# Kernel tuning notes

Measured on AMD Instinct MI355X. Metric: run time of the kernel, lower is better.

Reference implementation:

```python
import jax, jax.numpy as jnp
import numpy as np

D_IN = 256
DIMS = 256


def setup_inputs() -> dict:
    key = jax.random.key(0)
    k1, k2, k3, k4, k5 = jax.random.split(key, 5)
    B, Tq, Tk = 4, 512, 512
    query = jax.random.normal(k1, (B, Tq, D_IN), dtype=jnp.float32)
    value = jax.random.normal(k2, (B, Tk, D_IN), dtype=jnp.float32)
    # Dense(dims, use_bias=False) kernels (glorot-like scale) and AdditiveAttention scale vector
    Wq = jax.random.normal(k3, (D_IN, DIMS), dtype=jnp.float32) / np.sqrt(D_IN)
    Wv = jax.random.normal(k4, (D_IN, DIMS), dtype=jnp.float32) / np.sqrt(D_IN)
    scale = jax.random.normal(k5, (DIMS,), dtype=jnp.float32)
    return {"query": query, "value": value, "Wq": Wq, "Wv": Wv, "scale": scale}


def reference(query, value, Wq, Wv, scale):
    # q_proj: [B,Tq,d], k_proj: [B,Tk,d]; attention value = RAW value tensor (as in source)
    q = jnp.einsum("bqi,id->bqd", query, Wq)
    k = jnp.einsum("bki,id->bkd", value, Wv)
    # Additive (Bahdanau) scores: [B,Tq,Tk] via broadcast tanh then reduce with scale
    scores = jnp.einsum("bqkd,d->bqk", jnp.tanh(q[:, :, None, :] + k[:, None, :, :]), scale)
    attn = jax.nn.softmax(scores, axis=-1)  # masks are all-ones -> no-op
    out = jnp.einsum("bqk,bki->bqi", attn, value)
    return out, attn
```

## Files before the change

### kernel.cpp

```cpp
#include <hip/hip_runtime.h>

#define LOG2E 1.4426950408889634f
#define TWO_LOG2E 2.885390081777927f

__device__ __forceinline__ float fast_exp2(float x) { return __builtin_amdgcn_exp2f(x); }
__device__ __forceinline__ float fast_rcp(float x)  { return __builtin_amdgcn_rcpf(x); }

__device__ __forceinline__ void term2(float s0, float s1, float qx, float qy,
                                      float kx, float ky, float& acc) {
    const float A = fmaf(qx, kx, 1.f);
    const float B = fmaf(qy, ky, 1.f);
    acc = fmaf(fmaf(s1, A, s0 * B), fast_rcp(A * B), acc);
}

__global__ __launch_bounds__(256) void proj_kernel(
    const float* __restrict__ query, const float* __restrict__ value,
    const float* __restrict__ Wq, const float* __restrict__ Wv,
    float* __restrict__ eq, float* __restrict__ ek)
{
    __shared__ float in_lds[8 * 256];
    const int t = threadIdx.x;
    const int row0 = blockIdx.x * 8;
    const float* src; const float* W; float* dst;
    if (row0 < 2048) { src = query + (size_t)row0 * 256; W = Wq; dst = eq + (size_t)row0 * 256; }
    else { const int r = row0 - 2048; src = value + (size_t)r * 256; W = Wv; dst = ek + (size_t)r * 256; }

    const float4* s4 = (const float4*)src;
    float4* l4 = (float4*)in_lds;
    l4[t] = s4[t];
    l4[t + 256] = s4[t + 256];
    __syncthreads();

    float acc[8];
#pragma unroll
    for (int r = 0; r < 8; ++r) acc[r] = 0.f;

    for (int d = 0; d < 256; d += 4) {
        const float w0 = W[(d + 0) * 256 + t];
        const float w1 = W[(d + 1) * 256 + t];
        const float w2 = W[(d + 2) * 256 + t];
        const float w3 = W[(d + 3) * 256 + t];
#pragma unroll
        for (int r = 0; r < 8; ++r) {
            const float4 v = *(const float4*)&in_lds[r * 256 + d];
            acc[r] = fmaf(v.x, w0, acc[r]);
            acc[r] = fmaf(v.y, w1, acc[r]);
            acc[r] = fmaf(v.z, w2, acc[r]);
            acc[r] = fmaf(v.w, w3, acc[r]);
        }
    }
#pragma unroll
    for (int r = 0; r < 8; ++r) dst[r * 256 + t] = fast_exp2(acc[r] * TWO_LOG2E);
}

#define EK_ST 260
#define EQ_ST 260
#define SS_ST 520
#define PS_ST 520
__global__ __launch_bounds__(1024) void fused_kernel(
    const float* __restrict__ eq, const float* __restrict__ ek,
    const float* __restrict__ scale, const float* __restrict__ value,
    float* __restrict__ attn, float* __restrict__ out)
{
    __shared__ float ek_lds[64 * EK_ST];
    __shared__ float eq_lds[8 * EQ_ST];
    __shared__ float sc_lds[256];
    __shared__ float s_tile[8 * SS_ST];
    __shared__ float pslot[8 * PS_ST];
    __shared__ float inv_lds[8];

    const int t = threadIdx.x;
    const int w = t >> 6, lane = t & 63;
    const int oct = w >> 1, qh = w & 1;
    const int dd = lane >> 5, qp = (lane >> 4) & 1, kq = lane & 15;
    const int qt = blockIdx.x, b = blockIdx.y;
    const int q0 = qt * 8;

    const float4* ekb4 = (const float4*)(ek + (size_t)(b * 512) * 256);

    if (t < 512) {
        const int row = t >> 6, c = t & 63;
        const float4 v = ((const float4*)(eq + (size_t)(b * 512 + q0) * 256))[row * 64 + c];
        *(float4*)&eq_lds[row * EQ_ST + 4 * c] = v;
    } else if (t < 768) {
        sc_lds[t - 512] = -2.f * scale[t - 512];
    }
    {
#pragma unroll
        for (int l = 0; l < 4; ++l) {
            const int row = w + 16 * l;
            const int cc = (lane + (row >> 2)) & 63;
            *(float4*)&ek_lds[row * EK_ST + 4 * cc] = ekb4[(size_t)row * 64 + lane];
        }
    }
    __syncthreads();

    const int qr0 = 4 * qh + 2 * qp;
    const float* eqr0 = &eq_lds[(qr0 + 0) * EQ_ST];
    const float* eqr1 = &eq_lds[(qr0 + 1) * EQ_ST];

    for (int tt = 0; tt < 8; ++tt) {
        float a00 = 0.f, a01 = 0.f, a02 = 0.f, a03 = 0.f;
        float a10 = 0.f, a11 = 0.f, a12 = 0.f, a13 = 0.f;

#pragma unroll
        for (int it = 0; it < 4; ++it) {
            const int d = 32 * oct + 16 * dd + 4 * it;
            const float4 sv  = *(const float4*)&sc_lds[d];
            const float4 q0v = *(const float4*)&eqr0[d];
            const float4 q1v = *(const float4*)&eqr1[d];
            const int cc = 4 * (((d >> 2) + kq) & 63);
            const float4 k0 = *(const float4*)&ek_lds[(4 * kq + 0) * EK_ST + cc];
            const float4 k1 = *(const float4*)&ek_lds[(4 * kq + 1) * EK_ST + cc];
            const float4 k2 = *(const float4*)&ek_lds[(4 * kq + 2) * EK_ST + cc];
            const float4 k3 = *(const float4*)&ek_lds[(4 * kq + 3) * EK_ST + cc];

            term2(sv.x, sv.y, q0v.x, q0v.y, k0.x, k0.y, a00);
            term2(sv.x, sv.y, q0v.x, q0v.y, k1.x, k1.y, a01);
            term2(sv.x, sv.y, q0v.x, q0v.y, k2.x, k2.y, a02);
            term2(sv.x, sv.y, q0v.x, q0v.y, k3.x, k3.y, a03);
            term2(sv.x, sv.y, q1v.x, q1v.y, k0.x, k0.y, a10);
            term2(sv.x, sv.y, q1v.x, q1v.y, k1.x, k1.y, a11);
            term2(sv.x, sv.y, q1v.x, q1v.y, k2.x, k2.y, a12);
            term2(sv.x, sv.y, q1v.x, q1v.y, k3.x, k3.y, a13);

            term2(sv.z, sv.w, q0v.z, q0v.w, k0.z, k0.w, a00);
            term2(sv.z, sv.w, q0v.z, q0v.w, k1.z, k1.w, a01);
            term2(sv.z, sv.w, q0v.z, q0v.w, k2.z, k2.w, a02);
            term2(sv.z, sv.w, q0v.z, q0v.w, k3.z, k3.w, a03);
            term2(sv.z, sv.w, q1v.z, q1v.w, k0.z, k0.w, a10);
            term2(sv.z, sv.w, q1v.z, q1v.w, k1.z, k1.w, a11);
            term2(sv.z, sv.w, q1v.z, q1v.w, k2.z, k2.w, a12);
            term2(sv.z, sv.w, q1v.z, q1v.w, k3.z, k3.w, a13);
        }

        a00 += __shfl_xor(a00, 32); a01 += __shfl_xor(a01, 32);
        a02 += __shfl_xor(a02, 32); a03 += __shfl_xor(a03, 32);
        a10 += __shfl_xor(a10, 32); a11 += __shfl_xor(a11, 32);
        a12 += __shfl_xor(a12, 32); a13 += __shfl_xor(a13, 32);

        if (dd == 0) {
            float* ps = &pslot[oct * PS_ST];
            const int s0i = (qr0 + 0) * 64 + 4 * kq;
            const int s1i = (qr0 + 1) * 64 + 4 * kq;
            ps[s0i + 0] = a00; ps[s0i + 1] = a01; ps[s0i + 2] = a02; ps[s0i + 3] = a03;
            ps[s1i + 0] = a10; ps[s1i + 1] = a11; ps[s1i + 2] = a12; ps[s1i + 3] = a13;
        }
        __syncthreads();

        if (tt < 7) {
            const float4* src = ekb4 + (size_t)(64 * (tt + 1)) * 64;
#pragma unroll
            for (int l = 0; l < 4; ++l) {
                const int row = w + 16 * l;
                const int cc = (lane + (row >> 2)) & 63;
                *(float4*)&ek_lds[row * EK_ST + 4 * cc] = src[(size_t)row * 64 + lane];
            }
        }
        if (t < 512) {
            float s = pslot[t];
#pragma unroll
            for (int o = 1; o < 8; ++o) s += pslot[o * PS_ST + t];
            s_tile[(t >> 6) * SS_ST + 64 * tt + (t & 63)] = s;
        }
        __syncthreads();
    }

    if (w < 8) {
        float x[8];
        float m = -1e30f;
#pragma unroll
        for (int j = 0; j < 8; ++j) {
            x[j] = s_tile[w * SS_ST + 64 * j + lane];
            m = fmaxf(m, x[j]);
        }
#pragma unroll
        for (int off = 32; off; off >>= 1) m = fmaxf(m, __shfl_xor(m, off));

        float sum = 0.f;
#pragma unroll
        for (int j = 0; j < 8; ++j) { x[j] = fast_exp2((x[j] - m) * LOG2E); sum += x[j]; }
#pragma unroll
        for (int off = 32; off; off >>= 1) sum += __shfl_xor(sum, off);
        const float inv = fast_rcp(sum);

        float* arow = attn + (size_t)(b * 512 + q0 + w) * 512;
#pragma unroll
        for (int j = 0; j < 8; ++j) {
            s_tile[w * SS_ST + 64 * j + lane] = x[j];
            arow[64 * j + lane] = x[j] * inv;
        }
        if (lane == 0) inv_lds[w] = inv;
    }
    __syncthreads();

    float4 acc[8];
#pragma unroll
    for (int r = 0; r < 8; ++r) acc[r] = make_float4(0.f, 0.f, 0.f, 0.f);

    const float* vbase = value + (size_t)(b * 512 + 32 * w) * 256;
    for (int k4 = 0; k4 < 32; k4 += 4) {
        const float4 v0 = *(const float4*)&vbase[(k4 + 0) * 256 + lane * 4];
        const float4 v1 = *(const float4*)&vbase[(k4 + 1) * 256 + lane * 4];
        const float4 v2 = *(const float4*)&vbase[(k4 + 2) * 256 + lane * 4];
        const float4 v3 = *(const float4*)&vbase[(k4 + 3) * 256 + lane * 4];
#pragma unroll
        for (int r = 0; r < 8; ++r) {
            const float4 s4 = *(const float4*)&s_tile[r * SS_ST + 32 * w + k4];
            acc[r].x = fmaf(s4.x, v0.x, acc[r].x); acc[r].y = fmaf(s4.x, v0.y, acc[r].y);
            acc[r].z = fmaf(s4.x, v0.z, acc[r].z); acc[r].w = fmaf(s4.x, v0.w, acc[r].w);
            acc[r].x = fmaf(s4.y, v1.x, acc[r].x); acc[r].y = fmaf(s4.y, v1.y, acc[r].y);
            acc[r].z = fmaf(s4.y, v1.z, acc[r].z); acc[r].w = fmaf(s4.y, v1.w, acc[r].w);
            acc[r].x = fmaf(s4.z, v2.x, acc[r].x); acc[r].y = fmaf(s4.z, v2.y, acc[r].y);
            acc[r].z = fmaf(s4.z, v2.z, acc[r].z); acc[r].w = fmaf(s4.z, v2.w, acc[r].w);
            acc[r].x = fmaf(s4.w, v3.x, acc[r].x); acc[r].y = fmaf(s4.w, v3.y, acc[r].y);
            acc[r].z = fmaf(s4.w, v3.z, acc[r].z); acc[r].w = fmaf(s4.w, v3.w, acc[r].w);
        }
    }

    float* red = ek_lds;
    if (w >= 8) {
#pragma unroll
        for (int r = 0; r < 8; ++r)
            *(float4*)&red[((w - 8) * 8 + r) * 256 + lane * 4] = acc[r];
    }
    __syncthreads();
    if (w < 8) {
#pragma unroll
        for (int r = 0; r < 8; ++r) {
            const float4 o = *(const float4*)&red[(w * 8 + r) * 256 + lane * 4];
            acc[r].x += o.x; acc[r].y += o.y; acc[r].z += o.z; acc[r].w += o.w;
        }
    }
    __syncthreads();
    if (w >= 4 && w < 8) {
#pragma unroll
        for (int r = 0; r < 8; ++r)
            *(float4*)&red[((w - 4) * 8 + r) * 256 + lane * 4] = acc[r];
    }
    __syncthreads();
    if (w < 4) {
#pragma unroll
        for (int r = 0; r < 8; ++r) {
            const float4 o = *(const float4*)&red[(w * 8 + r) * 256 + lane * 4];
            acc[r].x += o.x; acc[r].y += o.y; acc[r].z += o.z; acc[r].w += o.w;
        }
    }
    __syncthreads();
    if (w >= 2 && w < 4) {
#pragma unroll
        for (int r = 0; r < 8; ++r)
            *(float4*)&red[((w - 2) * 8 + r) * 256 + lane * 4] = acc[r];
    }
    __syncthreads();
    if (w < 2) {
#pragma unroll
        for (int r = 0; r < 8; ++r) {
            const float4 o = *(const float4*)&red[(w * 8 + r) * 256 + lane * 4];
            acc[r].x += o.x; acc[r].y += o.y; acc[r].z += o.z; acc[r].w += o.w;
        }
    }
    __syncthreads();
    if (w == 1) {
#pragma unroll
        for (int r = 0; r < 8; ++r)
            *(float4*)&red[r * 256 + lane * 4] = acc[r];
    }
    __syncthreads();
    if (w == 0) {
#pragma unroll
        for (int r = 0; r < 8; ++r) {
            const float4 o = *(const float4*)&red[r * 256 + lane * 4];
            const float iv = inv_lds[r];
            float4 res;
            res.x = (acc[r].x + o.x) * iv;
            res.y = (acc[r].y + o.y) * iv;
            res.z = (acc[r].z + o.z) * iv;
            res.w = (acc[r].w + o.w) * iv;
            *(float4*)&out[(size_t)(b * 512 + q0 + r) * 256 + lane * 4] = res;
        }
    }
}

extern "C" void kernel_launch(void* const* d_in, const int* in_sizes, int n_in,
                              void* d_out, int out_size, void* d_ws, size_t ws_size,
                              hipStream_t stream) {
    const float* query = (const float*)d_in[0];
    const float* value = (const float*)d_in[1];
    const float* Wq    = (const float*)d_in[2];
    const float* Wv    = (const float*)d_in[3];
    const float* scale = (const float*)d_in[4];

    float* out0 = (float*)d_out;
    float* attn = out0 + 4 * 512 * 256;

    float* eq = (float*)d_ws;
    float* ek = eq + 2048 * 256;

    proj_kernel<<<512, 256, 0, stream>>>(query, value, Wq, Wv, eq, ek);
    fused_kernel<<<dim3(64, 4), 1024, 0, stream>>>(eq, ek, scale, value, attn, out0);
}
```

Baseline: 67.59 us.

## Prefetch next ek tile into registers and software-pipeline LDS loads in score loop

The global loads for the next 64-row ek tile are now issued at the start of each tt iteration into registers and only written to LDS after the barrier. This hides global memory latency behind the tanh-score compute. The inner d-loop is also double-buffered so the next step's LDS loads are issued before the current step's math. Launch bounds gain a min-blocks hint of 4, which constrains registers while the pipelining adds register pressure, so spills or occupancy loss are possible.

```diff
diff --git a/kernel.cpp b/kernel.cpp
--- a/kernel.cpp
+++ b/kernel.cpp
@@ -57,7 +57,7 @@
 #define EQ_ST 260
 #define SS_ST 520
 #define PS_ST 520
-__global__ __launch_bounds__(1024) void fused_kernel(
+__global__ __launch_bounds__(1024, 4) void fused_kernel(
     const float* __restrict__ eq, const float* __restrict__ ek,
     const float* __restrict__ scale, const float* __restrict__ value,
     float* __restrict__ attn, float* __restrict__ out)
@@ -98,40 +98,66 @@
     const int qr0 = 4 * qh + 2 * qp;
     const float* eqr0 = &eq_lds[(qr0 + 0) * EQ_ST];
     const float* eqr1 = &eq_lds[(qr0 + 1) * EQ_ST];
+    const int d0 = 32 * oct + 16 * dd;
 
     for (int tt = 0; tt < 8; ++tt) {
+        float4 g0, g1, g2, g3;
+        if (tt < 7) {
+            const float4* src = ekb4 + (size_t)(64 * (tt + 1)) * 64;
+            g0 = src[(size_t)(w +  0) * 64 + lane];
+            g1 = src[(size_t)(w + 16) * 64 + lane];
+            g2 = src[(size_t)(w + 32) * 64 + lane];
+            g3 = src[(size_t)(w + 48) * 64 + lane];
+        }
+
         float a00 = 0.f, a01 = 0.f, a02 = 0.f, a03 = 0.f;
         float a10 = 0.f, a11 = 0.f, a12 = 0.f, a13 = 0.f;
 
+        float4 sv, q0v, q1v, k0, k1, k2, k3;
+        {
+            const int d = d0;
+            sv  = *(const float4*)&sc_lds[d];
+            q0v = *(const float4*)&eqr0[d];
+            q1v = *(const float4*)&eqr1[d];
+            const int cc = 4 * (((d >> 2) + kq) & 63);
+            k0 = *(const float4*)&ek_lds[(4 * kq + 0) * EK_ST + cc];
+            k1 = *(const float4*)&ek_lds[(4 * kq + 1) * EK_ST + cc];
+            k2 = *(const float4*)&ek_lds[(4 * kq + 2) * EK_ST + cc];
+            k3 = *(const float4*)&ek_lds[(4 * kq + 3) * EK_ST + cc];
+        }
 #pragma unroll
         for (int it = 0; it < 4; ++it) {
-            const int d = 32 * oct + 16 * dd + 4 * it;
-            const float4 sv  = *(const float4*)&sc_lds[d];
-            const float4 q0v = *(const float4*)&eqr0[d];
-            const float4 q1v = *(const float4*)&eqr1[d];
-            const int cc = 4 * (((d >> 2) + kq) & 63);
-            const float4 k0 = *(const float4*)&ek_lds[(4 * kq + 0) * EK_ST + cc];
-            const float4 k1 = *(const float4*)&ek_lds[(4 * kq + 1) * EK_ST + cc];
-            const float4 k2 = *(const float4*)&ek_lds[(4 * kq + 2) * EK_ST + cc];
-            const float4 k3 = *(const float4*)&ek_lds[(4 * kq + 3) * EK_ST + cc];
-
-            term2(sv.x, sv.y, q0v.x, q0v.y, k0.x, k0.y, a00);
-            term2(sv.x, sv.y, q0v.x, q0v.y, k1.x, k1.y, a01);
-            term2(sv.x, sv.y, q0v.x, q0v.y, k2.x, k2.y, a02);
-            term2(sv.x, sv.y, q0v.x, q0v.y, k3.x, k3.y, a03);
-            term2(sv.x, sv.y, q1v.x, q1v.y, k0.x, k0.y, a10);
-            term2(sv.x, sv.y, q1v.x, q1v.y, k1.x, k1.y, a11);
-            term2(sv.x, sv.y, q1v.x, q1v.y, k2.x, k2.y, a12);
-            term2(sv.x, sv.y, q1v.x, q1v.y, k3.x, k3.y, a13);
-
-            term2(sv.z, sv.w, q0v.z, q0v.w, k0.z, k0.w, a00);
-            term2(sv.z, sv.w, q0v.z, q0v.w, k1.z, k1.w, a01);
-            term2(sv.z, sv.w, q0v.z, q0v.w, k2.z, k2.w, a02);
-            term2(sv.z, sv.w, q0v.z, q0v.w, k3.z, k3.w, a03);
-            term2(sv.z, sv.w, q1v.z, q1v.w, k0.z, k0.w, a10);
-            term2(sv.z, sv.w, q1v.z, q1v.w, k1.z, k1.w, a11);
-            term2(sv.z, sv.w, q1v.z, q1v.w, k2.z, k2.w, a12);
-            term2(sv.z, sv.w, q1v.z, q1v.w, k3.z, k3.w, a13);
+            const float4 csv = sv, cq0 = q0v, cq1 = q1v;
+            const float4 ck0 = k0, ck1 = k1, ck2 = k2, ck3 = k3;
+            if (it < 3) {
+                const int d = d0 + 4 * (it + 1);
+                sv  = *(const float4*)&sc_lds[d];
+                q0v = *(const float4*)&eqr0[d];
+                q1v = *(const float4*)&eqr1[d];
+                const int cc = 4 * (((d >> 2) + kq) & 63);
+                k0 = *(const float4*)&ek_lds[(4 * kq + 0) * EK_ST + cc];
+                k1 = *(const float4*)&ek_lds[(4 * kq + 1) * EK_ST + cc];
+                k2 = *(const float4*)&ek_lds[(4 * kq + 2) * EK_ST + cc];
+                k3 = *(const float4*)&ek_lds[(4 * kq + 3) * EK_ST + cc];
+            }
+
+            term2(csv.x, csv.y, cq0.x, cq0.y, ck0.x, ck0.y, a00);
+            term2(csv.x, csv.y, cq0.x, cq0.y, ck1.x, ck1.y, a01);
+            term2(csv.x, csv.y, cq0.x, cq0.y, ck2.x, ck2.y, a02);
+            term2(csv.x, csv.y, cq0.x, cq0.y, ck3.x, ck3.y, a03);
+            term2(csv.x, csv.y, cq1.x, cq1.y, ck0.x, ck0.y, a10);
+            term2(csv.x, csv.y, cq1.x, cq1.y, ck1.x, ck1.y, a11);
+            term2(csv.x, csv.y, cq1.x, cq1.y, ck2.x, ck2.y, a12);
+            term2(csv.x, csv.y, cq1.x, cq1.y, ck3.x, ck3.y, a13);
+
+            term2(csv.z, csv.w, cq0.z, cq0.w, ck0.z, ck0.w, a00);
+            term2(csv.z, csv.w, cq0.z, cq0.w, ck1.z, ck1.w, a01);
+            term2(csv.z, csv.w, cq0.z, cq0.w, ck2.z, ck2.w, a02);
+            term2(csv.z, csv.w, cq0.z, cq0.w, ck3.z, ck3.w, a03);
+            term2(csv.z, csv.w, cq1.z, cq1.w, ck0.z, ck0.w, a10);
+            term2(csv.z, csv.w, cq1.z, cq1.w, ck1.z, ck1.w, a11);
+            term2(csv.z, csv.w, cq1.z, cq1.w, ck2.z, ck2.w, a12);
+            term2(csv.z, csv.w, cq1.z, cq1.w, ck3.z, ck3.w, a13);
         }
 
         a00 += __shfl_xor(a00, 32); a01 += __shfl_xor(a01, 32);
@@ -149,12 +175,12 @@
         __syncthreads();
 
         if (tt < 7) {
-            const float4* src = ekb4 + (size_t)(64 * (tt + 1)) * 64;
 #pragma unroll
             for (int l = 0; l < 4; ++l) {
                 const int row = w + 16 * l;
                 const int cc = (lane + (row >> 2)) & 63;
-                *(float4*)&ek_lds[row * EK_ST + 4 * cc] = src[(size_t)row * 64 + lane];
+                const float4 g = (l == 0) ? g0 : (l == 1) ? g1 : (l == 2) ? g2 : g3;
+                *(float4*)&ek_lds[row * EK_ST + 4 * cc] = g;
             }
         }
         if (t < 512) {
```

Measured after the change: 66.32 us. About the same (-1.9%).

## Use 4x4 register tile for score loop and prefetch next key tile early

Applied to the files above, without the earlier changes.

Each lane now computes a 4-query by 4-key block over 8 dimensions instead of 2x4 over 16 dimensions, which changes the register blocking and the cross-lane reduction, now two xor shuffles. The next key tile is loaded from global memory into registers before the compute phase and stored to LDS after the barrier, so load latency overlaps with compute. The partial-sum layout now uses padded strides with float4 stores, and launch bounds request a minimum of 4 waves per SIMD. This trades more register pressure and an extra shuffle stage for better operand reuse and hidden global latency.

```diff
diff --git a/kernel.cpp b/kernel.cpp
--- a/kernel.cpp
+++ b/kernel.cpp
@@ -56,8 +56,9 @@
 #define EK_ST 260
 #define EQ_ST 260
 #define SS_ST 520
-#define PS_ST 520
-__global__ __launch_bounds__(1024) void fused_kernel(
+#define PSQ_ST 68
+#define PSO_ST (8 * PSQ_ST)
+__global__ __launch_bounds__(1024, 4) void fused_kernel(
     const float* __restrict__ eq, const float* __restrict__ ek,
     const float* __restrict__ scale, const float* __restrict__ value,
     float* __restrict__ attn, float* __restrict__ out)
@@ -66,13 +67,13 @@
     __shared__ float eq_lds[8 * EQ_ST];
     __shared__ float sc_lds[256];
     __shared__ float s_tile[8 * SS_ST];
-    __shared__ float pslot[8 * PS_ST];
+    __shared__ float pslot[8 * PSO_ST];
     __shared__ float inv_lds[8];
 
     const int t = threadIdx.x;
     const int w = t >> 6, lane = t & 63;
     const int oct = w >> 1, qh = w & 1;
-    const int dd = lane >> 5, qp = (lane >> 4) & 1, kq = lane & 15;
+    const int dd = lane >> 4, kq = lane & 15;
     const int qt = blockIdx.x, b = blockIdx.y;
     const int q0 = qt * 8;
 
@@ -95,73 +96,80 @@
     }
     __syncthreads();
 
-    const int qr0 = 4 * qh + 2 * qp;
-    const float* eqr0 = &eq_lds[(qr0 + 0) * EQ_ST];
-    const float* eqr1 = &eq_lds[(qr0 + 1) * EQ_ST];
+    const int d0 = 32 * oct + 8 * dd;
 
     for (int tt = 0; tt < 8; ++tt) {
-        float a00 = 0.f, a01 = 0.f, a02 = 0.f, a03 = 0.f;
-        float a10 = 0.f, a11 = 0.f, a12 = 0.f, a13 = 0.f;
-
-#pragma unroll
-        for (int it = 0; it < 4; ++it) {
-            const int d = 32 * oct + 16 * dd + 4 * it;
-            const float4 sv  = *(const float4*)&sc_lds[d];
-            const float4 q0v = *(const float4*)&eqr0[d];
-            const float4 q1v = *(const float4*)&eqr1[d];
-            const int cc = 4 * (((d >> 2) + kq) & 63);
-            const float4 k0 = *(const float4*)&ek_lds[(4 * kq + 0) * EK_ST + cc];
-            const float4 k1 = *(const float4*)&ek_lds[(4 * kq + 1) * EK_ST + cc];
-            const float4 k2 = *(const float4*)&ek_lds[(4 * kq + 2) * EK_ST + cc];
-            const float4 k3 = *(const float4*)&ek_lds[(4 * kq + 3) * EK_ST + cc];
-
-            term2(sv.x, sv.y, q0v.x, q0v.y, k0.x, k0.y, a00);
-            term2(sv.x, sv.y, q0v.x, q0v.y, k1.x, k1.y, a01);
-            term2(sv.x, sv.y, q0v.x, q0v.y, k2.x, k2.y, a02);
-            term2(sv.x, sv.y, q0v.x, q0v.y, k3.x, k3.y, a03);
-            term2(sv.x, sv.y, q1v.x, q1v.y, k0.x, k0.y, a10);
-            term2(sv.x, sv.y, q1v.x, q1v.y, k1.x, k1.y, a11);
-            term2(sv.x, sv.y, q1v.x, q1v.y, k2.x, k2.y, a12);
-            term2(sv.x, sv.y, q1v.x, q1v.y, k3.x, k3.y, a13);
-
-            term2(sv.z, sv.w, q0v.z, q0v.w, k0.z, k0.w, a00);
-            term2(sv.z, sv.w, q0v.z, q0v.w, k1.z, k1.w, a01);
-            term2(sv.z, sv.w, q0v.z, q0v.w, k2.z, k2.w, a02);
-            term2(sv.z, sv.w, q0v.z, q0v.w, k3.z, k3.w, a03);
-            term2(sv.z, sv.w, q1v.z, q1v.w, k0.z, k0.w, a10);
-            term2(sv.z, sv.w, q1v.z, q1v.w, k1.z, k1.w, a11);
-            term2(sv.z, sv.w, q1v.z, q1v.w, k2.z, k2.w, a12);
-            term2(sv.z, sv.w, q1v.z, q1v.w, k3.z, k3.w, a13);
-        }
-
-        a00 += __shfl_xor(a00, 32); a01 += __shfl_xor(a01, 32);
-        a02 += __shfl_xor(a02, 32); a03 += __shfl_xor(a03, 32);
-        a10 += __shfl_xor(a10, 32); a11 += __shfl_xor(a11, 32);
-        a12 += __shfl_xor(a12, 32); a13 += __shfl_xor(a13, 32);
-
-        if (dd == 0) {
-            float* ps = &pslot[oct * PS_ST];
-            const int s0i = (qr0 + 0) * 64 + 4 * kq;
-            const int s1i = (qr0 + 1) * 64 + 4 * kq;
-            ps[s0i + 0] = a00; ps[s0i + 1] = a01; ps[s0i + 2] = a02; ps[s0i + 3] = a03;
-            ps[s1i + 0] = a10; ps[s1i + 1] = a11; ps[s1i + 2] = a12; ps[s1i + 3] = a13;
-        }
-        __syncthreads();
-
+        float4 g0, g1, g2, g3;
         if (tt < 7) {
             const float4* src = ekb4 + (size_t)(64 * (tt + 1)) * 64;
+            g0 = src[(size_t)(w +  0) * 64 + lane];
+            g1 = src[(size_t)(w + 16) * 64 + lane];
+            g2 = src[(size_t)(w + 32) * 64 + lane];
+            g3 = src[(size_t)(w + 48) * 64 + lane];
+        }
+
+        float acc[4][4];
+#pragma unroll
+        for (int i = 0; i < 4; ++i)
+#pragma unroll
+            for (int j = 0; j < 4; ++j) acc[i][j] = 0.f;
+
+#pragma unroll
+        for (int it = 0; it < 2; ++it) {
+            const int d = d0 + 4 * it;
+            const float4 sv = *(const float4*)&sc_lds[d];
+            float4 qv[4], kv[4];
+#pragma unroll
+            for (int i = 0; i < 4; ++i)
+                qv[i] = *(const float4*)&eq_lds[(4 * qh + i) * EQ_ST + d];
+            const int cc = 4 * (((d >> 2) + kq) & 63);
+#pragma unroll
+            for (int j = 0; j < 4; ++j)
+                kv[j] = *(const float4*)&ek_lds[(4 * kq + j) * EK_ST + cc];
+
+#pragma unroll
+            for (int i = 0; i < 4; ++i)
+#pragma unroll
+                for (int j = 0; j < 4; ++j) {
+                    term2(sv.x, sv.y, qv[i].x, qv[i].y, kv[j].x, kv[j].y, acc[i][j]);
+                    term2(sv.z, sv.w, qv[i].z, qv[i].w, kv[j].z, kv[j].w, acc[i][j]);
+                }
+        }
+
+#pragma unroll
+        for (int i = 0; i < 4; ++i)
+#pragma unroll
+            for (int j = 0; j < 4; ++j) {
+                acc[i][j] += __shfl_xor(acc[i][j], 16);
+                acc[i][j] += __shfl_xor(acc[i][j], 32);
+            }
+
+        if (dd == 0) {
+            float* ps = &pslot[oct * PSO_ST + (4 * qh) * PSQ_ST];
+#pragma unroll
+            for (int i = 0; i < 4; ++i) {
+                float4 v; v.x = acc[i][0]; v.y = acc[i][1];
+                v.z = acc[i][2]; v.w = acc[i][3];
+                *(float4*)&ps[i * PSQ_ST + 4 * kq] = v;
+            }
+        }
+        __syncthreads();
+
+        if (tt < 7) {
 #pragma unroll
             for (int l = 0; l < 4; ++l) {
                 const int row = w + 16 * l;
                 const int cc = (lane + (row >> 2)) & 63;
-                *(float4*)&ek_lds[row * EK_ST + 4 * cc] = src[(size_t)row * 64 + lane];
+                const float4 g = (l == 0) ? g0 : (l == 1) ? g1 : (l == 2) ? g2 : g3;
+                *(float4*)&ek_lds[row * EK_ST + 4 * cc] = g;
             }
         }
         if (t < 512) {
-            float s = pslot[t];
-#pragma unroll
-            for (int o = 1; o < 8; ++o) s += pslot[o * PS_ST + t];
-            s_tile[(t >> 6) * SS_ST + 64 * tt + (t & 63)] = s;
+            const int qrow = t >> 6, k = t & 63;
+            float s = pslot[qrow * PSQ_ST + k];
+#pragma unroll
+            for (int o = 1; o < 8; ++o) s += pslot[o * PSO_ST + qrow * PSQ_ST + k];
+            s_tile[qrow * SS_ST + 64 * tt + k] = s;
         }
         __syncthreads();
     }
```

After: 69.82 us. 1.03x slower.
